# Kernel tuning notes

Hardware: AMD Instinct MI355X
Metric: run time of the kernel (lower is better)

## Reference

```python
import jax, jax.numpy as jnp
import numpy as np

MUL = 16            # multiplicity of 0e and 1o irreps (in and out)
N_NODES = 10000
N_EDGES = 160000
EDGE_FDIM = 128
H_DIM = 128
WNUM = 4 * MUL * MUL  # 4 instructions x (16 u x 1 v x 16 w) = 1024 weights per edge


def setup_inputs() -> dict:
    key = jax.random.key(0)
    ks = jax.random.split(key, 6)
    x = jax.random.normal(ks[0], (N_NODES, 4 * MUL), dtype=jnp.float32)  # 16x0e + 16x1o -> dim 64
    edge_index = jax.random.randint(ks[1], (2, N_EDGES), 0, N_NODES, dtype=jnp.int32)
    edge_attr = jax.random.normal(ks[2], (N_EDGES, EDGE_FDIM), dtype=jnp.float32)
    edge_sh = jax.random.normal(ks[3], (N_EDGES, 4), dtype=jnp.float32)  # 1x0e + 1x1o
    fc_w1 = jax.random.normal(ks[4], (EDGE_FDIM, H_DIM), dtype=jnp.float32) / np.sqrt(EDGE_FDIM)
    fc_b1 = jnp.zeros((H_DIM,), jnp.float32)
    fc_w2 = jax.random.normal(ks[5], (H_DIM, WNUM), dtype=jnp.float32) / np.sqrt(H_DIM)
    fc_b2 = jnp.zeros((WNUM,), jnp.float32)
    return dict(x=x, edge_index=edge_index, edge_attr=edge_attr, edge_sh=edge_sh,
                fc_w1=fc_w1, fc_b1=fc_b1, fc_w2=fc_w2, fc_b2=fc_b2)


def _tensor_product(xe, edge_sh, w):
    """FullyConnectedTensorProduct('16x0e+16x1o', '1x0e+1x1o', '16x0e+16x1o'),
    shared_weights=False. Instructions (uvw, v=1):
      0e x 0e -> 0e ; 0e x 1o -> 1o ; 1o x 0e -> 1o ; 1o x 1o -> 0e (dot / sqrt(3)).
    Path alpha = 1/sqrt(fan_in) with fan_in = 2*MUL per output irrep (2 paths x 16x1)."""
    x0 = xe[:, :MUL]                          # [E, 16] scalars
    x1 = xe[:, MUL:].reshape(-1, MUL, 3)      # [E, 16, 3] vectors
    sh0 = edge_sh[:, 0:1]                     # [E, 1]
    sh1 = edge_sh[:, 1:4]                     # [E, 3]
    wp = w.reshape(-1, 4, MUL, MUL)           # [E, 4 paths, u, w]
    w00, w01, w10, w11 = wp[:, 0], wp[:, 1], wp[:, 2], wp[:, 3]
    alpha = 1.0 / np.sqrt(2.0 * MUL)
    dot = jnp.einsum('eum,em->eu', x1, sh1)   # 1o . 1o -> 0e
    out0 = alpha * (jnp.einsum('eu,euw->ew', x0 * sh0, w00)
                    + jnp.einsum('eu,euw->ew', dot, w11) / np.sqrt(3.0))  # [E, 16]
    out1 = alpha * (jnp.einsum('eu,euw,em->ewm', x0, w01, sh1)
                    + jnp.einsum('eum,euw->ewm', x1 * sh0[:, :, None], w10))  # [E, 16, 3]
    return jnp.concatenate([out0, out1.reshape(-1, 3 * MUL)], axis=-1)  # [E, 64]


def reference(x, edge_index, edge_attr, edge_sh, fc_w1, fc_b1, fc_w2, fc_b2):
    src, dst = edge_index[0], edge_index[1]
    # per-edge tensor-product weights from edge features (dropout p=0 -> identity)
    w = jax.nn.relu(edge_attr @ fc_w1 + fc_b1) @ fc_w2 + fc_b2       # [E, 1024]
    tp_out = _tensor_product(x[src], edge_sh, w)                      # gather + TP
    seg = jax.ops.segment_sum(tp_out, dst, num_segments=N_NODES)      # scatter-add
    cnt = jax.ops.segment_sum(jnp.ones((N_EDGES,), tp_out.dtype), dst, num_segments=N_NODES)
    out = seg / jnp.maximum(cnt, 1.0)[:, None]                        # mean aggregation
    # residual: out_dim == in_dim (64), so F.pad is a no-op
    return out + x
```

## Files before the change

kernel.cpp:

```cpp
#include <hip/hip_runtime.h>
#include <stdint.h>

#define E_TOTAL 160000
#define NODES   10000
#define FDIM    128
#define HDIM    128
#define WN      1024
#define CDIM    64
#define EPB     32
#define NTHR    256

typedef __bf16 bf16x8 __attribute__((ext_vector_type(8)));
typedef __bf16 bf16x4 __attribute__((ext_vector_type(4)));
typedef float  f32x4  __attribute__((ext_vector_type(4)));

#define MFMA16(a,b,c) __builtin_amdgcn_mfma_f32_16x16x32_bf16(a,b,c,0,0,0)

#define WS_W1B (512*1024)
#define WS_CNT (576*1024)

__device__ __forceinline__ f32x4 ntload4(const float* p) {
    return __builtin_nontemporal_load((const f32x4*)p);
}

__global__ void prep_kernel(const float* __restrict__ W1, const float* __restrict__ W2,
                            __bf16* __restrict__ W1B, __bf16* __restrict__ W2B,
                            float* __restrict__ out_acc, int* __restrict__ cnt) {
    const int b   = blockIdx.x;
    const int tid = threadIdx.x;
    if (b < 72) {
        const float* W = (b < 64) ? W2 : W1;
        __bf16* outB   = (b < 64) ? W2B : W1B;
        const int N    = (b < 64) ? WN : HDIM;
        const int tile = (b < 64) ? b : (b - 64);
        const int lane = tid & 63, ks = tid >> 6;
        const int n  = tile * 16 + (lane & 15);
        const int k0 = ks * 32 + (lane >> 4) * 8;
        bf16x8 hi;
        #pragma unroll
        for (int j = 0; j < 8; ++j) hi[j] = (__bf16)W[(size_t)(k0 + j) * N + n];
        *(bf16x8*)(outB + ((size_t)(tile * 4 + ks) * 64 + lane) * 8) = hi;
    } else {
        const int zt = (b - 72) * NTHR + tid;
        const float4 z4 = make_float4(0.f, 0.f, 0.f, 0.f);
        for (int i = zt; i < NODES * CDIM / 4; i += 8 * NTHR) ((float4*)out_acc)[i] = z4;
        for (int i = zt; i < NODES; i += 8 * NTHR) cnt[i] = 0;
    }
}

__global__ __launch_bounds__(NTHR, 4)
void fused_edge_kernel(const float* __restrict__ x,
                       const int*   __restrict__ edge_index,
                       const float* __restrict__ edge_attr,
                       const float* __restrict__ edge_sh,
                       const float* __restrict__ fc_b1,
                       const float* __restrict__ fc_b2,
                       const __bf16* __restrict__ W1B,
                       const __bf16* __restrict__ W2B,
                       float* __restrict__ out_acc,
                       int*   __restrict__ cnt)
{
    __shared__ __align__(16) char s_pool[32768];
    __shared__ float s_sh1[3][36];
    __shared__ int   s_dst[EPB];

    float*  s_f    = (float*)s_pool;
    __bf16* s_attr = (__bf16*)(s_pool + 12288);
    __bf16* s_h    = (__bf16*)(s_pool + 20480);
    float*  s_b2s  = (float*)(s_pool + 28672);

    const int tid  = threadIdx.x;
    const int w    = tid >> 6;
    const int th   = w >> 1;
    const int kh   = w & 1;
    const int lane = tid & 63;
    const int quad = lane >> 4;
    const int li   = lane & 15;
    const int e0   = blockIdx.x * EPB;

    if (lane < 32) {
        const int e  = lane;
        const int up = w * 4;
        const int ge = e0 + e;
        const int src = edge_index[ge];
        const f32x4 sh4 = ntload4(edge_sh + (size_t)ge * 4);
        if (tid < EPB) {
            const int d = edge_index[E_TOTAL + ge];
            s_dst[e] = d;
            atomicAdd(&cnt[d], 1);
            s_sh1[0][e] = sh4.y; s_sh1[1][e] = sh4.z; s_sh1[2][e] = sh4.w;
        }
        const float* xp = x + (size_t)src * CDIM;
        const float4 x0v = *(const float4*)(xp + up);
        const float4 xa  = *(const float4*)(xp + 16 + up * 3);
        const float4 xb  = *(const float4*)(xp + 16 + up * 3 + 4);
        const float4 xc  = *(const float4*)(xp + 16 + up * 3 + 8);
        const float x1v[4][3] = {
            {xa.x, xa.y, xa.z}, {xa.w, xb.x, xb.y},
            {xb.z, xb.w, xc.x}, {xc.y, xc.z, xc.w}};
        const float x0a[4] = {x0v.x, x0v.y, x0v.z, x0v.w};
        const float alpha = 0.17677669529663689f;
        const float ai3   = alpha * 0.57735026918962576f;
        const float sh0 = sh4.x;
        #pragma unroll
        for (int j = 0; j < 4; ++j) {
            const int u = up + j;
            const float x0u = x0a[j];
            s_f[(0 * 16 + u) * 32 + e] = alpha * sh0 * x0u;
            s_f[(1 * 16 + u) * 32 + e] = alpha * x0u;
            s_f[(2 * 16 + u) * 32 + e] = alpha * sh0 * x1v[j][0];
            s_f[(3 * 16 + u) * 32 + e] = alpha * sh0 * x1v[j][1];
            s_f[(4 * 16 + u) * 32 + e] = alpha * sh0 * x1v[j][2];
            s_f[(5 * 16 + u) * 32 + e] = ai3 * (x1v[j][0]*sh4.y + x1v[j][1]*sh4.z + x1v[j][2]*sh4.w);
        }
    }
    #pragma unroll
    for (int t4 = 0; t4 < 4; ++t4) {
        const int t = tid + t4 * NTHR;
        const int e = t >> 5, i4 = t & 31;
        const f32x4 v = ntload4(edge_attr + (size_t)(e0 + e) * FDIM + i4 * 4);
        const int f = i4 >> 3, j0 = (i4 & 1) * 4, qc = (i4 >> 1) & 3;
        const int g = e >> 4, lc = e & 15;
        bf16x4 bv = {(__bf16)v[0], (__bf16)v[1], (__bf16)v[2], (__bf16)v[3]};
        *(bf16x4*)(s_attr + (((f * 2 + g) * 64 + qc * 16 + lc) * 8 + j0)) = bv;
    }
    *(f32x4*)&s_b2s[tid * 4] = *(const f32x4*)(fc_b2 + tid * 4);
    __syncthreads();

    {
        const int nt0 = w * 2;
        const float b1a = fc_b1[nt0 * 16 + li];
        const float b1b = fc_b1[(nt0 + 1) * 16 + li];
        bf16x8 A1[2][4];
        #pragma unroll
        for (int g = 0; g < 2; ++g)
            #pragma unroll
            for (int ks = 0; ks < 4; ++ks)
                A1[g][ks] = *(const bf16x8*)(s_attr + ((ks * 2 + g) * 64 + lane) * 8);
        #pragma unroll
        for (int nt2 = 0; nt2 < 2; ++nt2) {
            const int nt = nt0 + nt2;
            const float bias = nt2 ? b1b : b1a;
            bf16x8 Bf[4];
            #pragma unroll
            for (int ks = 0; ks < 4; ++ks)
                Bf[ks] = *(const bf16x8*)(W1B + ((size_t)(nt * 4 + ks) * 64 + lane) * 8);
            f32x4 acc[2];
            #pragma unroll
            for (int g = 0; g < 2; ++g) acc[g] = (f32x4){bias, bias, bias, bias};
            #pragma unroll
            for (int ks = 0; ks < 4; ++ks)
                #pragma unroll
                for (int g = 0; g < 2; ++g) acc[g] = MFMA16(A1[g][ks], Bf[ks], acc[g]);
            const int f  = nt >> 1;
            const int qc = (2 * (nt & 1) + (li >> 3)) & 3;
            const int j  = li & 7;
            #pragma unroll
            for (int g = 0; g < 2; ++g)
                #pragma unroll
                for (int r = 0; r < 4; ++r)
                    s_h[((f * 2 + g) * 64 + qc * 16 + (quad * 4 + r)) * 8 + j] =
                        (__bf16)fmaxf(acc[g][r], 0.f);
        }
    }
    __syncthreads();

    bf16x8 A2[2][2];
    #pragma unroll
    for (int g = 0; g < 2; ++g)
        #pragma unroll
        for (int k2 = 0; k2 < 2; ++k2)
            A2[g][k2] = *(const bf16x8*)(s_h + (((kh * 2 + k2) * 2 + g) * 64 + lane) * 8);

    f32x4 o0[2];
    f32x4 o1[2][3];
    #pragma unroll
    for (int g = 0; g < 2; ++g) {
        o0[g] = (f32x4){0.f, 0.f, 0.f, 0.f};
        #pragma unroll
        for (int m = 0; m < 3; ++m) o1[g][m] = (f32x4){0.f, 0.f, 0.f, 0.f};
    }
    const int tbase = th * 32;
    const __bf16* Wp = W2B + ((size_t)(tbase * 4 + kh * 2) * 64 + lane) * 8;
    bf16x8 P[4][2];
    #pragma unroll
    for (int s = 0; s < 4; ++s)
        #pragma unroll
        for (int k2 = 0; k2 < 2; ++k2)
            P[s][k2] = *(const bf16x8*)(Wp + (s * 4 + k2) * 512);

    #pragma unroll
    for (int half = 0; half < 2; ++half) {
        #pragma unroll
        for (int cc = 0; cc < 16; ++cc) {
            const int c = half * 16 + cc;
            const int u = cc;
            const bf16x8 b0 = P[c & 3][0];
            const bf16x8 b1 = P[c & 3][1];
            if (c + 4 < 32) {
                #pragma unroll
                for (int k2 = 0; k2 < 2; ++k2)
                    P[c & 3][k2] = *(const bf16x8*)(Wp + ((c + 4) * 4 + k2) * 512);
            }
            f32x4 acc[2];
            if (kh == 0) {
                const float b2v = s_b2s[(tbase + c) * 16 + li];
                acc[0] = (f32x4){b2v, b2v, b2v, b2v};
                acc[1] = acc[0];
            } else {
                acc[0] = (f32x4){0.f, 0.f, 0.f, 0.f};
                acc[1] = acc[0];
            }
            #pragma unroll
            for (int g = 0; g < 2; ++g) {
                acc[g] = MFMA16(A2[g][0], b0, acc[g]);
                acc[g] = MFMA16(A2[g][1], b1, acc[g]);
            }
            if (th == 0) {
                if (half == 0) {
                    #pragma unroll
                    for (int g = 0; g < 2; ++g)
                        o0[g] += *(const f32x4*)&s_f[(0 * 16 + u) * 32 + g * 16 + quad * 4] * acc[g];
                } else {
                    #pragma unroll
                    for (int g = 0; g < 2; ++g)
                        o1[g][0] += *(const f32x4*)&s_f[(1 * 16 + u) * 32 + g * 16 + quad * 4] * acc[g];
                }
            } else {
                if (half == 0) {
                    #pragma unroll
                    for (int g = 0; g < 2; ++g)
                        #pragma unroll
                        for (int m = 0; m < 3; ++m)
                            o1[g][m] += *(const f32x4*)&s_f[((2 + m) * 16 + u) * 32 + g * 16 + quad * 4] * acc[g];
                } else {
                    #pragma unroll
                    for (int g = 0; g < 2; ++g)
                        o0[g] += *(const f32x4*)&s_f[(5 * 16 + u) * 32 + g * 16 + quad * 4] * acc[g];
                }
            }
        }
    }
    if (th == 0) {
        #pragma unroll
        for (int g = 0; g < 2; ++g) {
            const f32x4 t1 = o1[g][0];
            o1[g][2] = t1 * *(const f32x4*)&s_sh1[2][g * 16 + quad * 4];
            o1[g][1] = t1 * *(const f32x4*)&s_sh1[1][g * 16 + quad * 4];
            o1[g][0] = t1 * *(const f32x4*)&s_sh1[0][g * 16 + quad * 4];
        }
    }

    __syncthreads();
    float* dA = (float*)s_pool;
    float* dB = (float*)(s_pool + 8448);
    float* dC = (float*)(s_pool + 16896);
    float* dD = (float*)(s_pool + 19072);
    if (kh == 1) {
        float* base = (th == 0) ? dA : dB;
        #pragma unroll
        for (int g = 0; g < 2; ++g)
            #pragma unroll
            for (int r = 0; r < 4; ++r) {
                float* row = base + (g * 16 + quad * 4 + r) * 66;
                row[li] = o0[g][r];
                #pragma unroll
                for (int m = 0; m < 3; ++m) row[16 + li * 3 + m] = o1[g][m][r];
            }
    } else if (th == 1) {
        #pragma unroll
        for (int g = 0; g < 2; ++g)
            #pragma unroll
            for (int r = 0; r < 4; ++r)
                dC[(g * 16 + quad * 4 + r) * 17 + li] = o0[g][r];
    } else {
        #pragma unroll
        for (int g = 0; g < 2; ++g)
            #pragma unroll
            for (int r = 0; r < 4; ++r) {
                float* row = dD + (g * 16 + quad * 4 + r) * 49 + li * 3;
                row[0] = o1[g][0][r]; row[1] = o1[g][1][r]; row[2] = o1[g][2][r];
            }
    }
    __syncthreads();
    if (kh == 0 && th == 0) {
        #pragma unroll
        for (int g = 0; g < 2; ++g)
            #pragma unroll
            for (int r = 0; r < 4; ++r) {
                const int e = g * 16 + quad * 4 + r;
                const float v = o0[g][r] + dA[e * 66 + li] + dB[e * 66 + li] + dC[e * 17 + li];
                unsafeAtomicAdd(out_acc + (size_t)s_dst[e] * CDIM + li, v);
            }
    } else if (kh == 0 && th == 1) {
        #pragma unroll
        for (int g = 0; g < 2; ++g)
            #pragma unroll
            for (int r = 0; r < 4; ++r) {
                const int e = g * 16 + quad * 4 + r;
                float* op = out_acc + (size_t)s_dst[e] * CDIM + 16 + li * 3;
                const float* rA = dA + e * 66 + 16 + li * 3;
                const float* rB = dB + e * 66 + 16 + li * 3;
                const float* rD = dD + e * 49 + li * 3;
                #pragma unroll
                for (int m = 0; m < 3; ++m)
                    unsafeAtomicAdd(op + m, o1[g][m][r] + rA[m] + rB[m] + rD[m]);
            }
    }
}

__global__ void finalize_kernel(const float* __restrict__ x,
                                const int*   __restrict__ cnt,
                                float*       __restrict__ out)
{
    const int idx = blockIdx.x * blockDim.x + threadIdx.x;
    if (idx < NODES * CDIM) {
        const int n = idx >> 6;
        const float c = (float)(cnt[n] > 1 ? cnt[n] : 1);
        out[idx] = out[idx] / c + x[idx];
    }
}

extern "C" void kernel_launch(void* const* d_in, const int* in_sizes, int n_in,
                              void* d_out, int out_size, void* d_ws, size_t ws_size,
                              hipStream_t stream) {
    (void)in_sizes; (void)n_in; (void)out_size; (void)ws_size;
    const float* x          = (const float*)d_in[0];
    const int*   edge_index = (const int*)  d_in[1];
    const float* edge_attr  = (const float*)d_in[2];
    const float* edge_sh    = (const float*)d_in[3];
    const float* fc_w1      = (const float*)d_in[4];
    const float* fc_b1      = (const float*)d_in[5];
    const float* fc_w2      = (const float*)d_in[6];
    const float* fc_b2      = (const float*)d_in[7];
    float*  out = (float*)d_out;
    __bf16* W2B = (__bf16*)d_ws;
    __bf16* W1B = (__bf16*)((char*)d_ws + WS_W1B);
    int*    cnt = (int*)((char*)d_ws + WS_CNT);

    prep_kernel<<<80, NTHR, 0, stream>>>(fc_w1, fc_w2, W1B, W2B, out, cnt);
    fused_edge_kernel<<<E_TOTAL / EPB, NTHR, 0, stream>>>(
        x, edge_index, edge_attr, edge_sh, fc_b1, fc_b2, W1B, W2B, out, cnt);
    finalize_kernel<<<(NODES * CDIM + NTHR - 1) / NTHR, NTHR, 0, stream>>>(x, cnt, out);
}
```

Measured before the change: 253.3 us.

## Process two edge tiles per block with register prefetch of next tile

Each block now handles two 32-edge tiles in a loop. The edge_attr, edge_sh and index loads for the next tile are issued into registers before the second GEMM of the current tile, so global-memory latency can overlap with MFMA work. This halves the grid size and amortises the b2 bias load, but it raises register pressure and adds a block-wide sync between tiles.

```diff
diff --git a/kernel.cpp b/kernel.cpp
--- a/kernel.cpp
+++ b/kernel.cpp
@@ -8,6 +8,7 @@
 #define WN      1024
 #define CDIM    64
 #define EPB     32
+#define TPB     2
 #define NTHR    256
 
 typedef __bf16 bf16x8 __attribute__((ext_vector_type(8)));
@@ -76,236 +77,274 @@
     const int lane = tid & 63;
     const int quad = lane >> 4;
     const int li   = lane & 15;
-    const int e0   = blockIdx.x * EPB;
-
-    if (lane < 32) {
-        const int e  = lane;
-        const int up = w * 4;
-        const int ge = e0 + e;
-        const int src = edge_index[ge];
-        const f32x4 sh4 = ntload4(edge_sh + (size_t)ge * 4);
-        if (tid < EPB) {
-            const int d = edge_index[E_TOTAL + ge];
-            s_dst[e] = d;
-            atomicAdd(&cnt[d], 1);
-            s_sh1[0][e] = sh4.y; s_sh1[1][e] = sh4.z; s_sh1[2][e] = sh4.w;
-        }
-        const float* xp = x + (size_t)src * CDIM;
-        const float4 x0v = *(const float4*)(xp + up);
-        const float4 xa  = *(const float4*)(xp + 16 + up * 3);
-        const float4 xb  = *(const float4*)(xp + 16 + up * 3 + 4);
-        const float4 xc  = *(const float4*)(xp + 16 + up * 3 + 8);
-        const float x1v[4][3] = {
-            {xa.x, xa.y, xa.z}, {xa.w, xb.x, xb.y},
-            {xb.z, xb.w, xc.x}, {xc.y, xc.z, xc.w}};
-        const float x0a[4] = {x0v.x, x0v.y, x0v.z, x0v.w};
-        const float alpha = 0.17677669529663689f;
-        const float ai3   = alpha * 0.57735026918962576f;
-        const float sh0 = sh4.x;
-        #pragma unroll
-        for (int j = 0; j < 4; ++j) {
-            const int u = up + j;
-            const float x0u = x0a[j];
-            s_f[(0 * 16 + u) * 32 + e] = alpha * sh0 * x0u;
-            s_f[(1 * 16 + u) * 32 + e] = alpha * x0u;
-            s_f[(2 * 16 + u) * 32 + e] = alpha * sh0 * x1v[j][0];
-            s_f[(3 * 16 + u) * 32 + e] = alpha * sh0 * x1v[j][1];
-            s_f[(4 * 16 + u) * 32 + e] = alpha * sh0 * x1v[j][2];
-            s_f[(5 * 16 + u) * 32 + e] = ai3 * (x1v[j][0]*sh4.y + x1v[j][1]*sh4.z + x1v[j][2]*sh4.w);
-        }
+    const int e0b  = blockIdx.x * (EPB * TPB);
+
+    f32x4 at_pf0, at_pf1, at_pf2, at_pf3;
+    f32x4 sh_pf = {0.f, 0.f, 0.f, 0.f};
+    int   src_pf = 0, dst_pf = 0;
+
+    {
+        const int e0 = e0b;
+        if (lane < 32) {
+            const int ge = e0 + lane;
+            src_pf = edge_index[ge];
+            sh_pf  = ntload4(edge_sh + (size_t)ge * 4);
+            if (tid < EPB) dst_pf = edge_index[E_TOTAL + ge];
+        }
+        const float* ap = edge_attr + (size_t)e0 * FDIM;
+        at_pf0 = ntload4(ap + (tid + 0 * NTHR) * 4);
+        at_pf1 = ntload4(ap + (tid + 1 * NTHR) * 4);
+        at_pf2 = ntload4(ap + (tid + 2 * NTHR) * 4);
+        at_pf3 = ntload4(ap + (tid + 3 * NTHR) * 4);
     }
+
     #pragma unroll
-    for (int t4 = 0; t4 < 4; ++t4) {
-        const int t = tid + t4 * NTHR;
-        const int e = t >> 5, i4 = t & 31;
-        const f32x4 v = ntload4(edge_attr + (size_t)(e0 + e) * FDIM + i4 * 4);
-        const int f = i4 >> 3, j0 = (i4 & 1) * 4, qc = (i4 >> 1) & 3;
-        const int g = e >> 4, lc = e & 15;
-        bf16x4 bv = {(__bf16)v[0], (__bf16)v[1], (__bf16)v[2], (__bf16)v[3]};
-        *(bf16x4*)(s_attr + (((f * 2 + g) * 64 + qc * 16 + lc) * 8 + j0)) = bv;
-    }
-    *(f32x4*)&s_b2s[tid * 4] = *(const f32x4*)(fc_b2 + tid * 4);
-    __syncthreads();
-
-    {
-        const int nt0 = w * 2;
-        const float b1a = fc_b1[nt0 * 16 + li];
-        const float b1b = fc_b1[(nt0 + 1) * 16 + li];
-        bf16x8 A1[2][4];
+    for (int t = 0; t < TPB; ++t) {
+        if (lane < 32) {
+            const int e  = lane;
+            const int up = w * 4;
+            const float* xp = x + (size_t)src_pf * CDIM;
+            const float4 x0v = *(const float4*)(xp + up);
+            const float4 xa  = *(const float4*)(xp + 16 + up * 3);
+            const float4 xb  = *(const float4*)(xp + 16 + up * 3 + 4);
+            const float4 xc  = *(const float4*)(xp + 16 + up * 3 + 8);
+            if (tid < EPB) {
+                s_dst[e] = dst_pf;
+                atomicAdd(&cnt[dst_pf], 1);
+                s_sh1[0][e] = sh_pf.y; s_sh1[1][e] = sh_pf.z; s_sh1[2][e] = sh_pf.w;
+            }
+            const float x1v[4][3] = {
+                {xa.x, xa.y, xa.z}, {xa.w, xb.x, xb.y},
+                {xb.z, xb.w, xc.x}, {xc.y, xc.z, xc.w}};
+            const float x0a[4] = {x0v.x, x0v.y, x0v.z, x0v.w};
+            const float alpha = 0.17677669529663689f;
+            const float ai3   = alpha * 0.57735026918962576f;
+            const float sh0 = sh_pf.x;
+            #pragma unroll
+            for (int j = 0; j < 4; ++j) {
+                const int u = up + j;
+                const float x0u = x0a[j];
+                s_f[(0 * 16 + u) * 32 + e] = alpha * sh0 * x0u;
+                s_f[(1 * 16 + u) * 32 + e] = alpha * x0u;
+                s_f[(2 * 16 + u) * 32 + e] = alpha * sh0 * x1v[j][0];
+                s_f[(3 * 16 + u) * 32 + e] = alpha * sh0 * x1v[j][1];
+                s_f[(4 * 16 + u) * 32 + e] = alpha * sh0 * x1v[j][2];
+                s_f[(5 * 16 + u) * 32 + e] = ai3 * (x1v[j][0]*sh_pf.y + x1v[j][1]*sh_pf.z + x1v[j][2]*sh_pf.w);
+            }
+        }
+        {
+            const f32x4 av[4] = {at_pf0, at_pf1, at_pf2, at_pf3};
+            #pragma unroll
+            for (int t4 = 0; t4 < 4; ++t4) {
+                const int tt = tid + t4 * NTHR;
+                const int e = tt >> 5, i4 = tt & 31;
+                const int f = i4 >> 3, j0 = (i4 & 1) * 4, qc = (i4 >> 1) & 3;
+                const int g = e >> 4, lc = e & 15;
+                const f32x4 v = av[t4];
+                bf16x4 bv = {(__bf16)v[0], (__bf16)v[1], (__bf16)v[2], (__bf16)v[3]};
+                *(bf16x4*)(s_attr + (((f * 2 + g) * 64 + qc * 16 + lc) * 8 + j0)) = bv;
+            }
+        }
+        if (t == 0)
+            *(f32x4*)&s_b2s[tid * 4] = *(const f32x4*)(fc_b2 + tid * 4);
+        __syncthreads();
+
+        {
+            const int nt0 = w * 2;
+            const float b1a = fc_b1[nt0 * 16 + li];
+            const float b1b = fc_b1[(nt0 + 1) * 16 + li];
+            bf16x8 A1[2][4];
+            #pragma unroll
+            for (int g = 0; g < 2; ++g)
+                #pragma unroll
+                for (int ks = 0; ks < 4; ++ks)
+                    A1[g][ks] = *(const bf16x8*)(s_attr + ((ks * 2 + g) * 64 + lane) * 8);
+            #pragma unroll
+            for (int nt2 = 0; nt2 < 2; ++nt2) {
+                const int nt = nt0 + nt2;
+                const float bias = nt2 ? b1b : b1a;
+                bf16x8 Bf[4];
+                #pragma unroll
+                for (int ks = 0; ks < 4; ++ks)
+                    Bf[ks] = *(const bf16x8*)(W1B + ((size_t)(nt * 4 + ks) * 64 + lane) * 8);
+                f32x4 acc[2];
+                #pragma unroll
+                for (int g = 0; g < 2; ++g) acc[g] = (f32x4){bias, bias, bias, bias};
+                #pragma unroll
+                for (int ks = 0; ks < 4; ++ks)
+                    #pragma unroll
+                    for (int g = 0; g < 2; ++g) acc[g] = MFMA16(A1[g][ks], Bf[ks], acc[g]);
+                const int f  = nt >> 1;
+                const int qc = (2 * (nt & 1) + (li >> 3)) & 3;
+                const int j  = li & 7;
+                #pragma unroll
+                for (int g = 0; g < 2; ++g)
+                    #pragma unroll
+                    for (int r = 0; r < 4; ++r)
+                        s_h[((f * 2 + g) * 64 + qc * 16 + (quad * 4 + r)) * 8 + j] =
+                            (__bf16)fmaxf(acc[g][r], 0.f);
+            }
+        }
+        __syncthreads();
+
+        bf16x8 A2[2][2];
         #pragma unroll
         for (int g = 0; g < 2; ++g)
             #pragma unroll
-            for (int ks = 0; ks < 4; ++ks)
-                A1[g][ks] = *(const bf16x8*)(s_attr + ((ks * 2 + g) * 64 + lane) * 8);
-        #pragma unroll
-        for (int nt2 = 0; nt2 < 2; ++nt2) {
-            const int nt = nt0 + nt2;
-            const float bias = nt2 ? b1b : b1a;
-            bf16x8 Bf[4];
-            #pragma unroll
-            for (int ks = 0; ks < 4; ++ks)
-                Bf[ks] = *(const bf16x8*)(W1B + ((size_t)(nt * 4 + ks) * 64 + lane) * 8);
-            f32x4 acc[2];
-            #pragma unroll
-            for (int g = 0; g < 2; ++g) acc[g] = (f32x4){bias, bias, bias, bias};
-            #pragma unroll
-            for (int ks = 0; ks < 4; ++ks)
-                #pragma unroll
-                for (int g = 0; g < 2; ++g) acc[g] = MFMA16(A1[g][ks], Bf[ks], acc[g]);
-            const int f  = nt >> 1;
-            const int qc = (2 * (nt & 1) + (li >> 3)) & 3;
-            const int j  = li & 7;
+            for (int k2 = 0; k2 < 2; ++k2)
+                A2[g][k2] = *(const bf16x8*)(s_h + (((kh * 2 + k2) * 2 + g) * 64 + lane) * 8);
+
+        if (t + 1 < TPB) {
+            const int e0n = e0b + (t + 1) * EPB;
+            if (lane < 32) {
+                const int ge = e0n + lane;
+                src_pf = edge_index[ge];
+                sh_pf  = ntload4(edge_sh + (size_t)ge * 4);
+                if (tid < EPB) dst_pf = edge_index[E_TOTAL + ge];
+            }
+            const float* ap = edge_attr + (size_t)e0n * FDIM;
+            at_pf0 = ntload4(ap + (tid + 0 * NTHR) * 4);
+            at_pf1 = ntload4(ap + (tid + 1 * NTHR) * 4);
+            at_pf2 = ntload4(ap + (tid + 2 * NTHR) * 4);
+            at_pf3 = ntload4(ap + (tid + 3 * NTHR) * 4);
+        }
+
+        f32x4 o0[2];
+        f32x4 o1[2][3];
+        #pragma unroll
+        for (int g = 0; g < 2; ++g) {
+            o0[g] = (f32x4){0.f, 0.f, 0.f, 0.f};
+            #pragma unroll
+            for (int m = 0; m < 3; ++m) o1[g][m] = (f32x4){0.f, 0.f, 0.f, 0.f};
+        }
+        const int tbase = th * 32;
+        const __bf16* Wp = W2B + ((size_t)(tbase * 4 + kh * 2) * 64 + lane) * 8;
+        bf16x8 P[4][2];
+        #pragma unroll
+        for (int s = 0; s < 4; ++s)
+            #pragma unroll
+            for (int k2 = 0; k2 < 2; ++k2)
+                P[s][k2] = *(const bf16x8*)(Wp + (s * 4 + k2) * 512);
+
+        #pragma unroll
+        for (int half = 0; half < 2; ++half) {
+            #pragma unroll
+            for (int cc = 0; cc < 16; ++cc) {
+                const int c = half * 16 + cc;
+                const int u = cc;
+                const bf16x8 b0 = P[c & 3][0];
+                const bf16x8 b1 = P[c & 3][1];
+                if (c + 4 < 32) {
+                    #pragma unroll
+                    for (int k2 = 0; k2 < 2; ++k2)
+                        P[c & 3][k2] = *(const bf16x8*)(Wp + ((c + 4) * 4 + k2) * 512);
+                }
+                f32x4 acc[2];
+                if (kh == 0) {
+                    const float b2v = s_b2s[(tbase + c) * 16 + li];
+                    acc[0] = (f32x4){b2v, b2v, b2v, b2v};
+                    acc[1] = acc[0];
+                } else {
+                    acc[0] = (f32x4){0.f, 0.f, 0.f, 0.f};
+                    acc[1] = acc[0];
+                }
+                #pragma unroll
+                for (int g = 0; g < 2; ++g) {
+                    acc[g] = MFMA16(A2[g][0], b0, acc[g]);
+                    acc[g] = MFMA16(A2[g][1], b1, acc[g]);
+                }
+                if (th == 0) {
+                    if (half == 0) {
+                        #pragma unroll
+                        for (int g = 0; g < 2; ++g)
+                            o0[g] += *(const f32x4*)&s_f[(0 * 16 + u) * 32 + g * 16 + quad * 4] * acc[g];
+                    } else {
+                        #pragma unroll
+                        for (int g = 0; g < 2; ++g)
+                            o1[g][0] += *(const f32x4*)&s_f[(1 * 16 + u) * 32 + g * 16 + quad * 4] * acc[g];
+                    }
+                } else {
+                    if (half == 0) {
+                        #pragma unroll
+                        for (int g = 0; g < 2; ++g)
+                            #pragma unroll
+                            for (int m = 0; m < 3; ++m)
+                                o1[g][m] += *(const f32x4*)&s_f[((2 + m) * 16 + u) * 32 + g * 16 + quad * 4] * acc[g];
+                    } else {
+                        #pragma unroll
+                        for (int g = 0; g < 2; ++g)
+                            o0[g] += *(const f32x4*)&s_f[(5 * 16 + u) * 32 + g * 16 + quad * 4] * acc[g];
+                    }
+                }
+            }
+        }
+        if (th == 0) {
+            #pragma unroll
+            for (int g = 0; g < 2; ++g) {
+                const f32x4 t1 = o1[g][0];
+                o1[g][2] = t1 * *(const f32x4*)&s_sh1[2][g * 16 + quad * 4];
+                o1[g][1] = t1 * *(const f32x4*)&s_sh1[1][g * 16 + quad * 4];
+                o1[g][0] = t1 * *(const f32x4*)&s_sh1[0][g * 16 + quad * 4];
+            }
+        }
+
+        __syncthreads();
+        float* dA = (float*)s_pool;
+        float* dB = (float*)(s_pool + 8448);
+        float* dC = (float*)(s_pool + 16896);
+        float* dD = (float*)(s_pool + 19072);
+        if (kh == 1) {
+            float* base = (th == 0) ? dA : dB;
+            #pragma unroll
+            for (int g = 0; g < 2; ++g)
+                #pragma unroll
+                for (int r = 0; r < 4; ++r) {
+                    float* row = base + (g * 16 + quad * 4 + r) * 66;
+                    row[li] = o0[g][r];
+                    #pragma unroll
+                    for (int m = 0; m < 3; ++m) row[16 + li * 3 + m] = o1[g][m][r];
+                }
+        } else if (th == 1) {
             #pragma unroll
             for (int g = 0; g < 2; ++g)
                 #pragma unroll
                 for (int r = 0; r < 4; ++r)
-                    s_h[((f * 2 + g) * 64 + qc * 16 + (quad * 4 + r)) * 8 + j] =
-                        (__bf16)fmaxf(acc[g][r], 0.f);
-        }
-    }
-    __syncthreads();
-
-    bf16x8 A2[2][2];
-    #pragma unroll
-    for (int g = 0; g < 2; ++g)
-        #pragma unroll
-        for (int k2 = 0; k2 < 2; ++k2)
-            A2[g][k2] = *(const bf16x8*)(s_h + (((kh * 2 + k2) * 2 + g) * 64 + lane) * 8);
-
-    f32x4 o0[2];
-    f32x4 o1[2][3];
-    #pragma unroll
-    for (int g = 0; g < 2; ++g) {
-        o0[g] = (f32x4){0.f, 0.f, 0.f, 0.f};
-        #pragma unroll
-        for (int m = 0; m < 3; ++m) o1[g][m] = (f32x4){0.f, 0.f, 0.f, 0.f};
-    }
-    const int tbase = th * 32;
-    const __bf16* Wp = W2B + ((size_t)(tbase * 4 + kh * 2) * 64 + lane) * 8;
-    bf16x8 P[4][2];
-    #pragma unroll
-    for (int s = 0; s < 4; ++s)
-        #pragma unroll
-        for (int k2 = 0; k2 < 2; ++k2)
-            P[s][k2] = *(const bf16x8*)(Wp + (s * 4 + k2) * 512);
-
-    #pragma unroll
-    for (int half = 0; half < 2; ++half) {
-        #pragma unroll
-        for (int cc = 0; cc < 16; ++cc) {
-            const int c = half * 16 + cc;
-            const int u = cc;
-            const bf16x8 b0 = P[c & 3][0];
-            const bf16x8 b1 = P[c & 3][1];
-            if (c + 4 < 32) {
-                #pragma unroll
-                for (int k2 = 0; k2 < 2; ++k2)
-                    P[c & 3][k2] = *(const bf16x8*)(Wp + ((c + 4) * 4 + k2) * 512);
-            }
-            f32x4 acc[2];
-            if (kh == 0) {
-                const float b2v = s_b2s[(tbase + c) * 16 + li];
-                acc[0] = (f32x4){b2v, b2v, b2v, b2v};
-                acc[1] = acc[0];
-            } else {
-                acc[0] = (f32x4){0.f, 0.f, 0.f, 0.f};
-                acc[1] = acc[0];
-            }
-            #pragma unroll
-            for (int g = 0; g < 2; ++g) {
-                acc[g] = MFMA16(A2[g][0], b0, acc[g]);
-                acc[g] = MFMA16(A2[g][1], b1, acc[g]);
-            }
-            if (th == 0) {
-                if (half == 0) {
-                    #pragma unroll
-                    for (int g = 0; g < 2; ++g)
-                        o0[g] += *(const f32x4*)&s_f[(0 * 16 + u) * 32 + g * 16 + quad * 4] * acc[g];
-                } else {
-                    #pragma unroll
-                    for (int g = 0; g < 2; ++g)
-                        o1[g][0] += *(const f32x4*)&s_f[(1 * 16 + u) * 32 + g * 16 + quad * 4] * acc[g];
-                }
-            } else {
-                if (half == 0) {
-                    #pragma unroll
-                    for (int g = 0; g < 2; ++g)
-                        #pragma unroll
-                        for (int m = 0; m < 3; ++m)
-                            o1[g][m] += *(const f32x4*)&s_f[((2 + m) * 16 + u) * 32 + g * 16 + quad * 4] * acc[g];
-                } else {
-                    #pragma unroll
-                    for (int g = 0; g < 2; ++g)
-                        o0[g] += *(const f32x4*)&s_f[(5 * 16 + u) * 32 + g * 16 + quad * 4] * acc[g];
-                }
-            }
-        }
-    }
-    if (th == 0) {
-        #pragma unroll
-        for (int g = 0; g < 2; ++g) {
-            const f32x4 t1 = o1[g][0];
-            o1[g][2] = t1 * *(const f32x4*)&s_sh1[2][g * 16 + quad * 4];
-            o1[g][1] = t1 * *(const f32x4*)&s_sh1[1][g * 16 + quad * 4];
-            o1[g][0] = t1 * *(const f32x4*)&s_sh1[0][g * 16 + quad * 4];
-        }
-    }
-
-    __syncthreads();
-    float* dA = (float*)s_pool;
-    float* dB = (float*)(s_pool + 8448);
-    float* dC = (float*)(s_pool + 16896);
-    float* dD = (float*)(s_pool + 19072);
-    if (kh == 1) {
-        float* base = (th == 0) ? dA : dB;
-        #pragma unroll
-        for (int g = 0; g < 2; ++g)
-            #pragma unroll
-            for (int r = 0; r < 4; ++r) {
-                float* row = base + (g * 16 + quad * 4 + r) * 66;
-                row[li] = o0[g][r];
-                #pragma unroll
-                for (int m = 0; m < 3; ++m) row[16 + li * 3 + m] = o1[g][m][r];
-            }
-    } else if (th == 1) {
-        #pragma unroll
-        for (int g = 0; g < 2; ++g)
-            #pragma unroll
-            for (int r = 0; r < 4; ++r)
-                dC[(g * 16 + quad * 4 + r) * 17 + li] = o0[g][r];
-    } else {
-        #pragma unroll
-        for (int g = 0; g < 2; ++g)
-            #pragma unroll
-            for (int r = 0; r < 4; ++r) {
-                float* row = dD + (g * 16 + quad * 4 + r) * 49 + li * 3;
-                row[0] = o1[g][0][r]; row[1] = o1[g][1][r]; row[2] = o1[g][2][r];
-            }
-    }
-    __syncthreads();
-    if (kh == 0 && th == 0) {
-        #pragma unroll
-        for (int g = 0; g < 2; ++g)
-            #pragma unroll
-            for (int r = 0; r < 4; ++r) {
-                const int e = g * 16 + quad * 4 + r;
-                const float v = o0[g][r] + dA[e * 66 + li] + dB[e * 66 + li] + dC[e * 17 + li];
-                unsafeAtomicAdd(out_acc + (size_t)s_dst[e] * CDIM + li, v);
-            }
-    } else if (kh == 0 && th == 1) {
-        #pragma unroll
-        for (int g = 0; g < 2; ++g)
-            #pragma unroll
-            for (int r = 0; r < 4; ++r) {
-                const int e = g * 16 + quad * 4 + r;
-                float* op = out_acc + (size_t)s_dst[e] * CDIM + 16 + li * 3;
-                const float* rA = dA + e * 66 + 16 + li * 3;
-                const float* rB = dB + e * 66 + 16 + li * 3;
-                const float* rD = dD + e * 49 + li * 3;
-                #pragma unroll
-                for (int m = 0; m < 3; ++m)
-                    unsafeAtomicAdd(op + m, o1[g][m][r] + rA[m] + rB[m] + rD[m]);
-            }
+                    dC[(g * 16 + quad * 4 + r) * 17 + li] = o0[g][r];
+        } else {
+            #pragma unroll
+            for (int g = 0; g < 2; ++g)
+                #pragma unroll
+                for (int r = 0; r < 4; ++r) {
+                    float* row = dD + (g * 16 + quad * 4 + r) * 49 + li * 3;
+                    row[0] = o1[g][0][r]; row[1] = o1[g][1][r]; row[2] = o1[g][2][r];
+                }
+        }
+        __syncthreads();
+        if (kh == 0 && th == 0) {
+            #pragma unroll
+            for (int g = 0; g < 2; ++g)
+                #pragma unroll
+                for (int r = 0; r < 4; ++r) {
+                    const int e = g * 16 + quad * 4 + r;
+                    const float v = o0[g][r] + dA[e * 66 + li] + dB[e * 66 + li] + dC[e * 17 + li];
+                    unsafeAtomicAdd(out_acc + (size_t)s_dst[e] * CDIM + li, v);
+                }
+        } else if (kh == 0 && th == 1) {
+            #pragma unroll
+            for (int g = 0; g < 2; ++g)
+                #pragma unroll
+                for (int r = 0; r < 4; ++r) {
+                    const int e = g * 16 + quad * 4 + r;
+                    float* op = out_acc + (size_t)s_dst[e] * CDIM + 16 + li * 3;
+                    const float* rA = dA + e * 66 + 16 + li * 3;
+                    const float* rB = dB + e * 66 + 16 + li * 3;
+                    const float* rD = dD + e * 49 + li * 3;
+                    #pragma unroll
+                    for (int m = 0; m < 3; ++m)
+                        unsafeAtomicAdd(op + m, o1[g][m][r] + rA[m] + rB[m] + rD[m]);
+                }
+        }
+        if (t + 1 < TPB) __syncthreads();
     }
 }
 
@@ -339,7 +378,7 @@
     int*    cnt = (int*)((char*)d_ws + WS_CNT);
 
     prep_kernel<<<80, NTHR, 0, stream>>>(fc_w1, fc_w2, W1B, W2B, out, cnt);
-    fused_edge_kernel<<<E_TOTAL / EPB, NTHR, 0, stream>>>(
+    fused_edge_kernel<<<E_TOTAL / (EPB * TPB), NTHR, 0, stream>>>(
         x, edge_index, edge_attr, edge_sh, fc_b1, fc_b2, W1B, W2B, out, cnt);
     finalize_kernel<<<(NODES * CDIM + NTHR - 1) / NTHR, NTHR, 0, stream>>>(x, cnt, out);
 }
```

Result: slower. 334.8 us (+32.1%).
